# Optimization experiments

Hardware: AMD Instinct MI355X
Metric: run time of the kernel (lower is better)

## Reference

```python
import jax, jax.numpy as jnp
import numpy as np

B, G, C, H = 32, 512, 384, 768
TAU = 0.1
ITERS = 10


def _xavier(key, shape):
    fan_in, fan_out = shape
    lim = (6.0 / (fan_in + fan_out)) ** 0.5
    return jax.random.uniform(key, shape, minval=-lim, maxval=lim, dtype=jnp.float32)


def setup_inputs() -> dict:
    key = jax.random.key(0)
    ks = jax.random.split(key, 4)
    return {
        "center_coords": jax.random.normal(ks[0], (B, G, 3), dtype=jnp.float32),
        "group_features": jax.random.normal(ks[1], (B, G, C), dtype=jnp.float32),
        "W1": _xavier(ks[2], (C, H)),
        "b1": jnp.zeros((H,), jnp.float32),
        "W2": _xavier(ks[3], (H, G)),
        "b2": jnp.zeros((G,), jnp.float32),
    }


def _sinkhorn(scores):
    # scores: (B, G, G); log-space Sinkhorn row/col normalization
    log_alpha = scores / TAU
    for _ in range(ITERS):
        log_alpha = log_alpha - jax.nn.logsumexp(log_alpha, axis=-1, keepdims=True)
        log_alpha = log_alpha - jax.nn.logsumexp(log_alpha, axis=-2, keepdims=True)
    return jnp.exp(log_alpha)


def _greedy_assign(P):
    # Equivalent to torch loop: process entries in descending value order,
    # assign (row, col) if both free == repeatedly take global argmax over
    # entries with free row and free col. P: (G, G) -> perm: (G,) int32.
    g = P.shape[-1]
    flat = P.reshape(-1)

    def step(_, carry):
        row_free, col_free, assign = carry
        mask = (row_free[:, None] & col_free[None, :]).reshape(-1)
        idx = jnp.argmax(jnp.where(mask, flat, -jnp.inf))
        r = idx // g
        c = idx % g
        return (row_free.at[r].set(False), col_free.at[c].set(False), assign.at[r].set(c.astype(jnp.int32)))

    init = (jnp.ones((g,), bool), jnp.ones((g,), bool), jnp.full((g,), -1, jnp.int32))
    _, _, assign = jax.lax.fori_loop(0, g, step, init)
    return assign


def _apply_perm(data, perm):
    # reordered[new_pos] = data[orig_pos]; perm[orig_pos] = new_pos
    return jnp.zeros_like(data).at[perm].set(data)


def reference(center_coords, group_features, W1, b1, W2, b2):
    h = jax.nn.relu(jnp.einsum('bgc,ch->bgh', group_features, W1) + b1)
    scores = jnp.einsum('bgh,hk->bgk', h, W2) + b2  # (B, G, G)
    P = _sinkhorn(scores)
    perm_indices = jax.vmap(_greedy_assign)(P)  # (B, G)
    reordered_coords = jax.vmap(_apply_perm)(center_coords, perm_indices)
    reordered_feats = jax.vmap(_apply_perm)(group_features, perm_indices)
    return reordered_coords, reordered_feats, perm_indices
```

## Files before the change

### kernel.cpp

```cpp
#include <hip/hip_runtime.h>
#include <math.h>

#define NB 32
#define NG 512
#define NC 384
#define NH 768

typedef float f32x4v __attribute__((ext_vector_type(4)));
typedef __bf16 bf16_t;
typedef bf16_t bf16x8 __attribute__((ext_vector_type(8)));
typedef bf16_t bf16x4 __attribute__((ext_vector_type(4)));

#define LDSK 32

__device__ __forceinline__ void split3(float x, bf16_t& h, bf16_t& m, bf16_t& lo)
{
    h = (bf16_t)x;
    float r1 = x - (float)h;
    m = (bf16_t)r1;
    float r2 = r1 - (float)m;
    lo = (bf16_t)r2;
}

__global__ __launch_bounds__(256, 4) void gemm_bias_mfma(
    const float* __restrict__ A, const float* __restrict__ Bw,
    const float* __restrict__ bias, float* __restrict__ Co,
    int M, int N, int K, int mode)
{
    __shared__ __align__(16) bf16_t sA[3][128][LDSK];
    __shared__ __align__(16) bf16_t sB[3][64][LDSK];
    int ntiles = N >> 6;
    int bm = (blockIdx.x / ntiles) << 7;
    int bn = (blockIdx.x % ntiles) << 6;
    int t = threadIdx.x;
    int l = t & 63;
    int w = t >> 6;
    int wr = (w >> 1) << 6;
    int wc = (w & 1) << 5;
    int fr = l & 15;
    int fq = l >> 4;

    int sa_row = t >> 1;
    int sa_kh = (t & 1) << 4;
    int hsel = (sa_kh >> 4) << 2;
    int aswz = (sa_row >> 1) & 3;
    int sb_k = (t & 7) << 2;
    int sb_n = ((t >> 3) & 15) << 2;
    bool doB = t < 128;
    int bslot = (sb_k >> 2) & 3;
    int bsub = (sb_k >> 4) << 2;

    const float* apBase = A + (size_t)(bm + sa_row) * K + sa_kh;

    f32x4v acc[4][2];
#pragma unroll
    for (int i = 0; i < 4; i++)
#pragma unroll
        for (int j = 0; j < 2; j++) acc[i][j] = (f32x4v)(0.f);

    float4 q0 = *(const float4*)(apBase + 0);
    float4 q1 = *(const float4*)(apBase + 4);
    float4 q2 = *(const float4*)(apBase + 8);
    float4 q3 = *(const float4*)(apBase + 12);
    float4 bq0, bq1, bq2, bq3;
    if (doB) {
        bq0 = *(const float4*)(Bw + (size_t)(sb_k + 0) * N + bn + sb_n);
        bq1 = *(const float4*)(Bw + (size_t)(sb_k + 1) * N + bn + sb_n);
        bq2 = *(const float4*)(Bw + (size_t)(sb_k + 2) * N + bn + sb_n);
        bq3 = *(const float4*)(Bw + (size_t)(sb_k + 3) * N + bn + sb_n);
    }

    for (int kc = 0; kc < K; kc += 32) {
        __syncthreads();
        {
            float xs[16] = { q0.x, q0.y, q0.z, q0.w, q1.x, q1.y, q1.z, q1.w,
                             q2.x, q2.y, q2.z, q2.w, q3.x, q3.y, q3.z, q3.w };
            bf16_t hs[16], ms[16], ls[16];
#pragma unroll
            for (int e = 0; e < 16; e++) split3(xs[e], hs[e], ms[e], ls[e]);
#pragma unroll
            for (int qd = 0; qd < 4; qd++) {
                int col = ((qd ^ aswz) << 3) + hsel;
                *(bf16x4*)&sA[0][sa_row][col] =
                    (bf16x4){ hs[4 * qd], hs[4 * qd + 1], hs[4 * qd + 2], hs[4 * qd + 3] };
                *(bf16x4*)&sA[1][sa_row][col] =
                    (bf16x4){ ms[4 * qd], ms[4 * qd + 1], ms[4 * qd + 2], ms[4 * qd + 3] };
                *(bf16x4*)&sA[2][sa_row][col] =
                    (bf16x4){ ls[4 * qd], ls[4 * qd + 1], ls[4 * qd + 2], ls[4 * qd + 3] };
            }
        }
        if (doB) {
            float bbv[4][4] = {
                { bq0.x, bq0.y, bq0.z, bq0.w },
                { bq1.x, bq1.y, bq1.z, bq1.w },
                { bq2.x, bq2.y, bq2.z, bq2.w },
                { bq3.x, bq3.y, bq3.z, bq3.w } };
#pragma unroll
            for (int n = 0; n < 4; n++) {
                int rb = sb_n + n;
                int col = ((bslot ^ ((rb >> 1) & 3)) << 3) + bsub;
                bf16_t hb[4], mb[4], lb[4];
#pragma unroll
                for (int kk = 0; kk < 4; kk++) split3(bbv[kk][n], hb[kk], mb[kk], lb[kk]);
                *(bf16x4*)&sB[0][rb][col] = (bf16x4){ hb[0], hb[1], hb[2], hb[3] };
                *(bf16x4*)&sB[1][rb][col] = (bf16x4){ mb[0], mb[1], mb[2], mb[3] };
                *(bf16x4*)&sB[2][rb][col] = (bf16x4){ lb[0], lb[1], lb[2], lb[3] };
            }
        }
        __syncthreads();
        if (kc + 32 < K) {
            const float* ap = apBase + kc + 32;
            q0 = *(const float4*)(ap + 0);
            q1 = *(const float4*)(ap + 4);
            q2 = *(const float4*)(ap + 8);
            q3 = *(const float4*)(ap + 12);
            if (doB) {
                const float* bp = Bw + (size_t)(kc + 32 + sb_k) * N + bn + sb_n;
                bq0 = *(const float4*)(bp + 0 * N);
                bq1 = *(const float4*)(bp + 1 * N);
                bq2 = *(const float4*)(bp + 2 * N);
                bq3 = *(const float4*)(bp + 3 * N);
            }
        }
        bf16x8 afH[4], afM[4], afL[4], bfH[2], bfM[2], bfL[2];
#pragma unroll
        for (int i = 0; i < 4; i++) {
            int ra = wr + i * 16 + fr;
            int pk = ((fq ^ ((ra >> 1) & 3)) << 3);
            afH[i] = *(const bf16x8*)&sA[0][ra][pk];
            afM[i] = *(const bf16x8*)&sA[1][ra][pk];
            afL[i] = *(const bf16x8*)&sA[2][ra][pk];
        }
#pragma unroll
        for (int j = 0; j < 2; j++) {
            int rb = wc + j * 16 + fr;
            int pk = ((fq ^ ((rb >> 1) & 3)) << 3);
            bfH[j] = *(const bf16x8*)&sB[0][rb][pk];
            bfM[j] = *(const bf16x8*)&sB[1][rb][pk];
            bfL[j] = *(const bf16x8*)&sB[2][rb][pk];
        }
#pragma unroll
        for (int i = 0; i < 4; i++)
#pragma unroll
            for (int j = 0; j < 2; j++) {
                acc[i][j] = __builtin_amdgcn_mfma_f32_16x16x32_bf16(
                    afH[i], bfH[j], acc[i][j], 0, 0, 0);
                acc[i][j] = __builtin_amdgcn_mfma_f32_16x16x32_bf16(
                    afH[i], bfM[j], acc[i][j], 0, 0, 0);
                acc[i][j] = __builtin_amdgcn_mfma_f32_16x16x32_bf16(
                    afM[i], bfH[j], acc[i][j], 0, 0, 0);
                acc[i][j] = __builtin_amdgcn_mfma_f32_16x16x32_bf16(
                    afM[i], bfM[j], acc[i][j], 0, 0, 0);
                acc[i][j] = __builtin_amdgcn_mfma_f32_16x16x32_bf16(
                    afH[i], bfL[j], acc[i][j], 0, 0, 0);
                acc[i][j] = __builtin_amdgcn_mfma_f32_16x16x32_bf16(
                    afL[i], bfH[j], acc[i][j], 0, 0, 0);
            }
    }

    int orow = fq << 2;
#pragma unroll
    for (int j = 0; j < 2; j++) {
        int colg = bn + wc + j * 16 + fr;
        float bj = bias[colg];
#pragma unroll
        for (int i = 0; i < 4; i++) {
            int rowg = bm + wr + i * 16 + orow;
#pragma unroll
            for (int r = 0; r < 4; r++) {
                float val = acc[i][j][r] + bj;
                val = (mode == 0) ? fmaxf(val, 0.f) : val / 0.1f;
                Co[(size_t)(rowg + r) * N + colg] = val;
            }
        }
    }
}

#define DPP6_MAXF(x)                                                              \
    { int _t;                                                                     \
      _t = __builtin_amdgcn_update_dpp(__float_as_int(x), __float_as_int(x),      \
               0x111, 0xf, 0xf, false); x = fmaxf(x, __int_as_float(_t));         \
      _t = __builtin_amdgcn_update_dpp(__float_as_int(x), __float_as_int(x),      \
               0x112, 0xf, 0xf, false); x = fmaxf(x, __int_as_float(_t));         \
      _t = __builtin_amdgcn_update_dpp(__float_as_int(x), __float_as_int(x),      \
               0x114, 0xf, 0xf, false); x = fmaxf(x, __int_as_float(_t));         \
      _t = __builtin_amdgcn_update_dpp(__float_as_int(x), __float_as_int(x),      \
               0x118, 0xf, 0xf, false); x = fmaxf(x, __int_as_float(_t));         \
      _t = __builtin_amdgcn_update_dpp(__float_as_int(x), __float_as_int(x),      \
               0x142, 0xa, 0xf, false); x = fmaxf(x, __int_as_float(_t));         \
      _t = __builtin_amdgcn_update_dpp(__float_as_int(x), __float_as_int(x),      \
               0x143, 0xc, 0xf, false); x = fmaxf(x, __int_as_float(_t)); }

#define DPP6_ADDF(x)                                                              \
    { int _t;                                                                     \
      _t = __builtin_amdgcn_update_dpp(__float_as_int(x), __float_as_int(x),      \
               0x111, 0xf, 0xf, false); x = x + __int_as_float(_t);               \
      _t = __builtin_amdgcn_update_dpp(__float_as_int(x), __float_as_int(x),      \
               0x112, 0xf, 0xf, false); x = x + __int_as_float(_t);               \
      _t = __builtin_amdgcn_update_dpp(__float_as_int(x), __float_as_int(x),      \
               0x114, 0xf, 0xf, false); x = x + __int_as_float(_t);               \
      _t = __builtin_amdgcn_update_dpp(__float_as_int(x), __float_as_int(x),      \
               0x118, 0xf, 0xf, false); x = x + __int_as_float(_t);               \
      _t = __builtin_amdgcn_update_dpp(__float_as_int(x), __float_as_int(x),      \
               0x142, 0xa, 0xf, false); x = x + __int_as_float(_t);               \
      _t = __builtin_amdgcn_update_dpp(__float_as_int(x), __float_as_int(x),      \
               0x143, 0xc, 0xf, false); x = x + __int_as_float(_t); }

__global__ __launch_bounds__(256) void sinkhorn_iter_fused(
    const float* __restrict__ A0, float* __restrict__ uu,
    const float* __restrict__ vIn, float* __restrict__ vOut,
    const float* __restrict__ psIn, float* __restrict__ psOut, int first)
{
    int blk = blockIdx.x;
    int b = blk >> 3, rc = blk & 7;
    int t = threadIdx.x;
    int l = t & 63, w = t >> 6;
    __shared__ __align__(16) float svv[512];

    if (first) {
        svv[t] = 0.f;
        svv[256 + t] = 0.f;
    } else {
#pragma unroll
        for (int h2 = 0; h2 < 2; h2++) {
            int j = h2 * 256 + t;
            float S = 0.f;
#pragma unroll
            for (int r8 = 0; r8 < 8; r8++) S += psIn[((b << 3) + r8) * NG + j];
            float nv = vIn[(b << 9) + j] - __logf(S);
            svv[j] = nv;
            if (rc == 0) vOut[(b << 9) + j] = nv;
        }
    }
    __syncthreads();

    float4 v0 = *(const float4*)(&svv[4 * l]);
    float4 v1 = *(const float4*)(&svv[256 + 4 * l]);
    int row0 = (rc << 6) + (w << 4);
    const float* base = A0 + ((size_t)((b << 9) + row0) << 9);

    float cs0 = 0.f, cs1 = 0.f, cs2 = 0.f, cs3 = 0.f;
    float cs4 = 0.f, cs5 = 0.f, cs6 = 0.f, cs7 = 0.f;

    for (int rr = 0; rr < 16; ++rr) {
        const float* rowp = base + ((size_t)rr << 9);
        float4 a0 = *(const float4*)(rowp + 4 * l);
        float4 a1 = *(const float4*)(rowp + 256 + 4 * l);
        float x0 = a0.x + v0.x, x1 = a0.y + v0.y;
        float x2 = a0.z + v0.z, x3 = a0.w + v0.w;
        float x4 = a1.x + v1.x, x5 = a1.y + v1.y;
        float x6 = a1.z + v1.z, x7 = a1.w + v1.w;
        float m = fmaxf(fmaxf(fmaxf(x0, x1), fmaxf(x2, x3)),
                        fmaxf(fmaxf(x4, x5), fmaxf(x6, x7)));
        DPP6_MAXF(m)
        int mi = __builtin_amdgcn_readlane(__float_as_int(m), 63);
        m = __int_as_float(mi);
        float e0 = __expf(x0 - m), e1 = __expf(x1 - m);
        float e2 = __expf(x2 - m), e3 = __expf(x3 - m);
        float e4 = __expf(x4 - m), e5 = __expf(x5 - m);
        float e6 = __expf(x6 - m), e7 = __expf(x7 - m);
        float s = ((e0 + e1) + (e2 + e3)) + ((e4 + e5) + (e6 + e7));
        DPP6_ADDF(s)
        int si = __builtin_amdgcn_readlane(__float_as_int(s), 63);
        s = __int_as_float(si);
        float inv = 1.0f / s;
        cs0 += e0 * inv; cs1 += e1 * inv; cs2 += e2 * inv; cs3 += e3 * inv;
        cs4 += e4 * inv; cs5 += e5 * inv; cs6 += e6 * inv; cs7 += e7 * inv;
        if (l == 63) uu[(b << 9) + row0 + rr] = -(m + __logf(s));
    }

    __shared__ float sacc[4][512];
    float4 w0; w0.x = cs0; w0.y = cs1; w0.z = cs2; w0.w = cs3;
    float4 w1; w1.x = cs4; w1.y = cs5; w1.z = cs6; w1.w = cs7;
    *(float4*)&sacc[w][4 * l] = w0;
    *(float4*)&sacc[w][256 + 4 * l] = w1;
    __syncthreads();
    float pA = sacc[0][t] + sacc[1][t] + sacc[2][t] + sacc[3][t];
    float pB = sacc[0][256 + t] + sacc[1][256 + t] + sacc[2][256 + t] + sacc[3][256 + t];
    int o = ((b << 3) + rc) * NG;
    psOut[o + t] = pA;
    psOut[o + 256 + t] = pB;
}

__global__ __launch_bounds__(256) void col_combine_final(
    const float* __restrict__ psIn, const float* __restrict__ vIn,
    float* __restrict__ vOut)
{
    int tid = blockIdx.x * 256 + threadIdx.x;
    int b = tid >> 9, j = tid & 511;
    float S = 0.f;
#pragma unroll
    for (int r8 = 0; r8 < 8; r8++) S += psIn[((b << 3) + r8) * NG + j];
    vOut[tid] = vIn[tid] - __logf(S);
}

__device__ __forceinline__ void masked_row_argmax(
    const float* __restrict__ rowp, int l, unsigned int free8, int rr,
    float& outV, int& outF)
{
    float4 x0 = *(const float4*)(rowp + 8 * l);
    float4 x1 = *(const float4*)(rowp + 8 * l + 4);
    float q0 = (free8 & 1u)   ? x0.x : -1.0f;
    float q1 = (free8 & 2u)   ? x0.y : -1.0f;
    float q2 = (free8 & 4u)   ? x0.z : -1.0f;
    float q3 = (free8 & 8u)   ? x0.w : -1.0f;
    float q4 = (free8 & 16u)  ? x1.x : -1.0f;
    float q5 = (free8 & 32u)  ? x1.y : -1.0f;
    float q6 = (free8 & 64u)  ? x1.z : -1.0f;
    float q7 = (free8 & 128u) ? x1.w : -1.0f;
    float lm = fmaxf(fmaxf(fmaxf(q0, q1), fmaxf(q2, q3)),
                     fmaxf(fmaxf(q4, q5), fmaxf(q6, q7)));
    int sb = (rr << 9) + 8 * l;
    int lf = 0x7FFFFFFF;
    lf = (q7 == lm) ? sb + 7 : lf;
    lf = (q6 == lm) ? sb + 6 : lf;
    lf = (q5 == lm) ? sb + 5 : lf;
    lf = (q4 == lm) ? sb + 4 : lf;
    lf = (q3 == lm) ? sb + 3 : lf;
    lf = (q2 == lm) ? sb + 2 : lf;
    lf = (q1 == lm) ? sb + 1 : lf;
    lf = (q0 == lm) ? sb + 0 : lf;
    float gg = lm;
    DPP6_MAXF(gg)
    int ggi = __builtin_amdgcn_readlane(__float_as_int(gg), 63);
    float g1 = __int_as_float(ggi);
    unsigned long long tb = __ballot(lm == g1);
    int tl = __ffsll(tb) - 1;
    outV = g1;
    outF = __builtin_amdgcn_readlane(lf, tl);
}

__global__ __launch_bounds__(256) void p_rowmax(
    const float* __restrict__ A0, const float* __restrict__ uu,
    const float* __restrict__ vv, float* __restrict__ P,
    int* __restrict__ rbCr, int* __restrict__ rbCc,
    unsigned long long* __restrict__ freeRow,
    unsigned long long* __restrict__ freeCol,
    int* __restrict__ remaining)
{
    if (blockIdx.x == 0) {
        int t = threadIdx.x;
        freeRow[t] = ~0ULL;
        freeCol[t] = ~0ULL;
        if (t < NB) remaining[t] = NG;
    }
    int wrow = blockIdx.x * 4 + (threadIdx.x >> 6);
    int l = threadIdx.x & 63;
    int b = wrow >> 9;
    float ur = uu[wrow];
    const float* vb = vv + (b << 9);
    size_t ro = (size_t)wrow << 9;
    float4 a0 = *(const float4*)(A0 + ro + 8 * l);
    float4 a1 = *(const float4*)(A0 + ro + 8 * l + 4);
    float4 v0 = *(const float4*)(vb + 8 * l);
    float4 v1 = *(const float4*)(vb + 8 * l + 4);
    float p0 = expf(a0.x + ur + v0.x);
    float p1 = expf(a0.y + ur + v0.y);
    float p2 = expf(a0.z + ur + v0.z);
    float p3 = expf(a0.w + ur + v0.w);
    float p4 = expf(a1.x + ur + v1.x);
    float p5 = expf(a1.y + ur + v1.y);
    float p6 = expf(a1.z + ur + v1.z);
    float p7 = expf(a1.w + ur + v1.w);
    float4 o0; o0.x = p0; o0.y = p1; o0.z = p2; o0.w = p3;
    float4 o1; o1.x = p4; o1.y = p5; o1.z = p6; o1.w = p7;
    *(float4*)(P + ro + 8 * l) = o0;
    *(float4*)(P + ro + 8 * l + 4) = o1;
    float mv = fmaxf(fmaxf(fmaxf(p0, p1), fmaxf(p2, p3)),
                     fmaxf(fmaxf(p4, p5), fmaxf(p6, p7)));
    int cb = 8 * l;
    int f = 0x7FFFFFFF;
    f = (p7 == mv) ? cb + 7 : f;
    f = (p6 == mv) ? cb + 6 : f;
    f = (p5 == mv) ? cb + 5 : f;
    f = (p4 == mv) ? cb + 4 : f;
    f = (p3 == mv) ? cb + 3 : f;
    f = (p2 == mv) ? cb + 2 : f;
    f = (p1 == mv) ? cb + 1 : f;
    f = (p0 == mv) ? cb + 0 : f;
    float g = mv;
    DPP6_MAXF(g)
    int gi = __builtin_amdgcn_readlane(__float_as_int(g), 63);
    float gm = __int_as_float(gi);
    unsigned long long tb = __ballot(mv == gm);
    int tl = __ffsll(tb) - 1;
    int bestc = __builtin_amdgcn_readlane(f, tl);
    if (l == 0) { rbCr[wrow] = bestc; rbCc[wrow] = -1; }
}

__global__ __launch_bounds__(512) void mutual_round(
    const float* __restrict__ P, int* __restrict__ rbCr, int* __restrict__ rbCc,
    unsigned long long* __restrict__ freeRow,
    unsigned long long* __restrict__ freeCol,
    int* __restrict__ remaining, int* __restrict__ permInt)
{
    int b = blockIdx.x;
    if (remaining[b] == 0) return;
    int t = threadIdx.x;
    int l = t & 63;
    int w = t >> 6;
    const float* Pb = P + (size_t)b * NG * NG;

    __shared__ unsigned int fr[16], fc[16];
    __shared__ int sRC[NG];
    __shared__ int sCC[NG];
    __shared__ int freeList[NG];
    __shared__ int dirtyRows[NG];
    __shared__ int nFree, nDirtyRow, takeCnt;
    __shared__ int wCnt[8], wOff[8];

    if (t < 8) {
        unsigned long long x = freeRow[b * 8 + t];
        fr[2 * t] = (unsigned)x; fr[2 * t + 1] = (unsigned)(x >> 32);
    } else if (t < 16) {
        int i = t - 8;
        unsigned long long x = freeCol[b * 8 + i];
        fc[2 * i] = (unsigned)x; fc[2 * i + 1] = (unsigned)(x >> 32);
    }
    sRC[t] = rbCr[(b << 9) + t];
    sCC[t] = rbCc[(b << 9) + t];
    if (t == 0) { nDirtyRow = 0; takeCnt = 0; }
    __syncthreads();

    bool isFree = (fr[t >> 5] >> (t & 31)) & 1u;
    unsigned long long bm = __ballot(isFree);
    if (l == 0) wCnt[w] = __popcll(bm);
    if (isFree) {
        int c = sRC[t];
        if (!((fc[c >> 5] >> (c & 31)) & 1u)) {
            int d = atomicAdd(&nDirtyRow, 1);
            dirtyRows[d] = t;
        }
    }
    __syncthreads();
    if (t == 0) {
        int s = 0;
#pragma unroll
        for (int i = 0; i < 8; i++) { wOff[i] = s; s += wCnt[i]; }
        nFree = s;
    }
    __syncthreads();
    if (isFree) {
        int rank = __popcll(bm & ((1ULL << l) - 1ULL));
        freeList[wOff[w] + rank] = t;
    }
    __syncthreads();

    int nd = nDirtyRow;
    for (int d = w; d < nd; d += 8) {
        int r = dirtyRows[d];
        unsigned int free8 = (fc[l >> 2] >> ((l & 3) * 8)) & 0xFFu;
        float nv; int nf;
        masked_row_argmax(Pb + ((size_t)r << 9), l, free8, r, nv, nf);
        if (l == 0) {
            int c = nf & 511;
            sRC[r] = c;
            rbCr[(b << 9) + r] = c;
        }
    }
    __syncthreads();

    bool colFree = (fc[t >> 5] >> (t & 31)) & 1u;
    int cachedR = sCC[t];
    bool colDirty = colFree &&
        (cachedR < 0 || !((fr[cachedR >> 5] >> (cachedR & 31)) & 1u));
    if (colDirty) {
        float best = -1.f; int bestr = 0x7FFFFFFF;
        int nf2 = nFree;
        int i = 0;
        for (; i + 4 <= nf2; i += 4) {
            int r0 = freeList[i], r1 = freeList[i + 1];
            int r2 = freeList[i + 2], r3 = freeList[i + 3];
            float v0 = Pb[((size_t)r0 << 9) + t];
            float v1 = Pb[((size_t)r1 << 9) + t];
            float v2 = Pb[((size_t)r2 << 9) + t];
            float v3 = Pb[((size_t)r3 << 9) + t];
            if (v0 > best) { best = v0; bestr = r0; }
            if (v1 > best) { best = v1; bestr = r1; }
            if (v2 > best) { best = v2; bestr = r2; }
            if (v3 > best) { best = v3; bestr = r3; }
        }
        for (; i < nf2; ++i) {
            int ri = freeList[i];
            float vv2 = Pb[((size_t)ri << 9) + t];
            if (vv2 > best) { best = vv2; bestr = ri; }
        }
        sCC[t] = bestr;
        rbCc[(b << 9) + t] = bestr;
    }
    __syncthreads();

    if (colFree) {
        int r = sCC[t];
        if (r >= 0 && r < NG && sRC[r] == t) {
            permInt[(b << 9) + r] = t;
            atomicAnd(&fr[r >> 5], ~(1u << (r & 31)));
            atomicAnd(&fc[t >> 5], ~(1u << (t & 31)));
            atomicAdd(&takeCnt, 1);
        }
    }
    __syncthreads();
    if (t < 8) {
        freeRow[b * 8 + t] =
            ((unsigned long long)fr[2 * t + 1] << 32) | fr[2 * t];
    } else if (t < 16) {
        int i = t - 8;
        freeCol[b * 8 + i] =
            ((unsigned long long)fc[2 * i + 1] << 32) | fc[2 * i];
    }
    if (t == 0) remaining[b] = remaining[b] - takeCnt;
}

__global__ __launch_bounds__(64) void greedy_cleanup(
    const float* __restrict__ P,
    const unsigned long long* __restrict__ freeRow,
    const unsigned long long* __restrict__ freeCol,
    const int* __restrict__ remaining, int* __restrict__ permInt)
{
    int b = blockIdx.x;
    if (remaining[b] == 0) return;
    int l = threadIdx.x;
    const float* Pb = P + (size_t)b * NG * NG;

    unsigned long long wR = freeRow[b * 8 + (l >> 3)];
    unsigned int myRows = (unsigned int)((wR >> ((l & 7) * 8)) & 0xFF);
    unsigned long long wC = freeCol[b * 8 + (l >> 3)];
    unsigned int free8 = (unsigned int)((wC >> ((l & 7) * 8)) & 0xFF);

    float rv[8]; int rf[8];
#pragma unroll
    for (int k = 0; k < 8; k++) { rv[k] = -1.f; rf[k] = 0x7FFFFFFF; }

    int dmk = (int)myRows;
    unsigned long long act = __ballot(dmk != 0);
    while (act) {
        int src = __ffsll(act) - 1;
        int kk = __ffs(__builtin_amdgcn_readlane(dmk, src)) - 1;
        if (l == src) dmk &= ~(1 << kk);
        int rr = (src << 3) + kk;
        float nv; int nf;
        masked_row_argmax(Pb + ((size_t)rr << 9), l, free8, rr, nv, nf);
        bool upd = (l == src);
        rv[0] = (upd && kk == 0) ? nv : rv[0]; rf[0] = (upd && kk == 0) ? nf : rf[0];
        rv[1] = (upd && kk == 1) ? nv : rv[1]; rf[1] = (upd && kk == 1) ? nf : rf[1];
        rv[2] = (upd && kk == 2) ? nv : rv[2]; rf[2] = (upd && kk == 2) ? nf : rf[2];
        rv[3] = (upd && kk == 3) ? nv : rv[3]; rf[3] = (upd && kk == 3) ? nf : rf[3];
        rv[4] = (upd && kk == 4) ? nv : rv[4]; rf[4] = (upd && kk == 4) ? nf : rf[4];
        rv[5] = (upd && kk == 5) ? nv : rv[5]; rf[5] = (upd && kk == 5) ? nf : rf[5];
        rv[6] = (upd && kk == 6) ? nv : rv[6]; rf[6] = (upd && kk == 6) ? nf : rf[6];
        rv[7] = (upd && kk == 7) ? nv : rv[7]; rf[7] = (upd && kk == 7) ? nf : rf[7];
        act = __ballot(dmk != 0);
    }

    for (int step = 0; step < NG; ++step) {
        float mv = fmaxf(fmaxf(fmaxf(rv[0], rv[1]), fmaxf(rv[2], rv[3])),
                         fmaxf(fmaxf(rv[4], rv[5]), fmaxf(rv[6], rv[7])));
        int f = 0x7FFFFFFF;
        f = (rv[7] == mv) ? rf[7] : f;
        f = (rv[6] == mv) ? rf[6] : f;
        f = (rv[5] == mv) ? rf[5] : f;
        f = (rv[4] == mv) ? rf[4] : f;
        f = (rv[3] == mv) ? rf[3] : f;
        f = (rv[2] == mv) ? rf[2] : f;
        f = (rv[1] == mv) ? rf[1] : f;
        f = (rv[0] == mv) ? rf[0] : f;
        float g = mv;
        DPP6_MAXF(g)
        int gi = __builtin_amdgcn_readlane(__float_as_int(g), 63);
        float gm = __int_as_float(gi);
        if (gm < 0.f) break;
        unsigned long long tb = __ballot(mv == gm);
        int tl = __ffsll(tb) - 1;
        int bestf = __builtin_amdgcn_readlane(f, tl);
        int r = bestf >> 9, c = bestf & 511;
        if (l == 0) permInt[(b << 9) + r] = c;
        if (l == (c >> 3)) free8 &= ~(1u << (c & 7));
        int rl = r - (l << 3);
        int dm2 = 0;
#pragma unroll
        for (int k = 0; k < 8; k++) {
            bool alive = rv[k] >= 0.f;
            bool cm = ((rf[k] ^ c) & 511) == 0;
            bool taken = (rl == k);
            if (taken) rv[k] = -1.f;
            dm2 |= (alive && cm && !taken) ? (1 << k) : 0;
        }
        unsigned long long act2 = __ballot(dm2 != 0);
        while (act2) {
            int src = __ffsll(act2) - 1;
            int kk = __ffs(__builtin_amdgcn_readlane(dm2, src)) - 1;
            if (l == src) dm2 &= ~(1 << kk);
            int rr = (src << 3) + kk;
            float nv; int nf;
            masked_row_argmax(Pb + ((size_t)rr << 9), l, free8, rr, nv, nf);
            bool upd = (l == src);
            rv[0] = (upd && kk == 0) ? nv : rv[0]; rf[0] = (upd && kk == 0) ? nf : rf[0];
            rv[1] = (upd && kk == 1) ? nv : rv[1]; rf[1] = (upd && kk == 1) ? nf : rf[1];
            rv[2] = (upd && kk == 2) ? nv : rv[2]; rf[2] = (upd && kk == 2) ? nf : rf[2];
            rv[3] = (upd && kk == 3) ? nv : rv[3]; rf[3] = (upd && kk == 3) ? nf : rf[3];
            rv[4] = (upd && kk == 4) ? nv : rv[4]; rf[4] = (upd && kk == 4) ? nf : rf[4];
            rv[5] = (upd && kk == 5) ? nv : rv[5]; rf[5] = (upd && kk == 5) ? nf : rf[5];
            rv[6] = (upd && kk == 6) ? nv : rv[6]; rf[6] = (upd && kk == 6) ? nf : rf[6];
            rv[7] = (upd && kk == 7) ? nv : rv[7]; rf[7] = (upd && kk == 7) ? nf : rf[7];
            act2 = __ballot(dm2 != 0);
        }
    }
}

__global__ void scatter_all(const float* __restrict__ coords,
    const float* __restrict__ feats, const int* __restrict__ perm,
    float* __restrict__ dstCoords, float* __restrict__ dstFeats,
    float* __restrict__ permF)
{
    int tid = blockIdx.x * 256 + threadIdx.x;
    int rc = tid / 96;
    int q = tid - rc * 96;
    int b = rc >> 9;
    int p = perm[rc];
    const float4* s4 = (const float4*)(feats + (size_t)rc * NC);
    float4* d4 = (float4*)(dstFeats + ((size_t)(b << 9) + p) * NC);
    d4[q] = s4[q];
    if (q == 0) {
        permF[rc] = (float)p;
        size_t so = (size_t)rc * 3;
        size_t dd = ((size_t)(b << 9) + p) * 3;
        dstCoords[dd] = coords[so];
        dstCoords[dd + 1] = coords[so + 1];
        dstCoords[dd + 2] = coords[so + 2];
    }
}

extern "C" void kernel_launch(void* const* d_in, const int* in_sizes, int n_in,
                              void* d_out, int out_size, void* d_ws, size_t ws_size,
                              hipStream_t stream)
{
    const float* coords = (const float*)d_in[0];
    const float* feats  = (const float*)d_in[1];
    const float* W1 = (const float*)d_in[2];
    const float* b1 = (const float*)d_in[3];
    const float* W2 = (const float*)d_in[4];
    const float* b2 = (const float*)d_in[5];

    float* out = (float*)d_out;
    float* outCoords = out;
    float* outFeats  = out + (size_t)NB * NG * 3;
    float* outPerm   = out + (size_t)NB * NG * 3 + (size_t)NB * NG * NC;

    float* ws = (float*)d_ws;
    float* h   = ws;
    float* A0  = h + (size_t)NB * NG * NH;
    float* u   = A0 + (size_t)NB * NG * NG;
    float* vA  = u + NB * NG;
    float* ps0 = vA + NB * NG;
    float* ps1 = ps0 + NB * 8 * NG;
    int* rbCr  = (int*)(ps1 + NB * 8 * NG);
    int* rbCc  = rbCr + NB * NG;
    unsigned long long* freeRow = (unsigned long long*)(rbCc + NB * NG);
    unsigned long long* freeCol = freeRow + NB * 8;
    int* remaining = (int*)(freeCol + NB * 8);
    int* permInt   = remaining + 32;
    float* vB  = (float*)(permInt + NB * NG);

    const int M = NB * NG;

    gemm_bias_mfma<<<dim3((M / 128) * (NH / 64)), 256, 0, stream>>>(
        feats, W1, b1, h, M, NH, NC, 0);
    gemm_bias_mfma<<<dim3((M / 128) * (NG / 64)), 256, 0, stream>>>(
        h, W2, b2, A0, M, NG, NH, 1);

    hipMemsetAsync(vA, 0, (size_t)NB * NG * sizeof(float), stream);

    float* pbuf[2] = { ps0, ps1 };
    for (int i = 1; i <= 10; ++i) {
        const float* vin = (i % 2 == 0) ? vA : vB;
        float* vout      = (i % 2 == 0) ? vB : vA;
        const float* pin = pbuf[i & 1];
        float* pout      = pbuf[(i - 1) & 1];
        sinkhorn_iter_fused<<<dim3(NB * 8), 256, 0, stream>>>(
            A0, u, vin, vout, pin, pout, (i == 1) ? 1 : 0);
    }
    col_combine_final<<<dim3(M / 256), 256, 0, stream>>>(pbuf[1], vB, vA);

    float* P = h;
    p_rowmax<<<dim3(M / 4), 256, 0, stream>>>(A0, u, vA, P, rbCr, rbCc,
                                              freeRow, freeCol, remaining);

    for (int r = 0; r < 6; ++r)
        mutual_round<<<dim3(NB), 512, 0, stream>>>(P, rbCr, rbCc, freeRow,
                                                   freeCol, remaining, permInt);

    greedy_cleanup<<<dim3(NB), 64, 0, stream>>>(P, freeRow, freeCol,
                                                remaining, permInt);

    scatter_all<<<dim3((NB * NG * 96) / 256), 256, 0, stream>>>(
        coords, feats, permInt, outCoords, outFeats, outPerm);
}
```

Measured before the change: 403.0 us.

## Pre-split weights into swizzled bf16 planes and shrink GEMM tile to 64x64

Adds a presplit_W kernel that converts W1/W2 once per call into three bf16 planes (hi/mid/lo) already in the swizzled LDS layout. The GEMM then copies B tiles straight into shared memory instead of loading fp32 and splitting them in every block. The M tile also shrinks from 128 to 64 rows, giving twice as many blocks with fewer accumulators each. The cost is two extra small launches, extra workspace for the planes, and more redundant reads of A across column tiles.

```diff
diff --git a/kernel.cpp b/kernel.cpp
--- a/kernel.cpp
+++ b/kernel.cpp
@@ -10,8 +10,6 @@
 typedef __bf16 bf16_t;
 typedef bf16_t bf16x8 __attribute__((ext_vector_type(8)));
 typedef bf16_t bf16x4 __attribute__((ext_vector_type(4)));
-
-#define LDSK 32
 
 __device__ __forceinline__ void split3(float x, bf16_t& h, bf16_t& m, bf16_t& lo)
 {
@@ -22,111 +20,111 @@
     lo = (bf16_t)r2;
 }
 
+__global__ __launch_bounds__(256) void presplit_W(
+    const float* __restrict__ W, bf16_t* __restrict__ planeB, int K, int N)
+{
+    int tid = blockIdx.x * 256 + threadIdx.x;
+    int nkc = K >> 5;
+    if (tid >= nkc * N) return;
+    int kc = tid / N;
+    int col = tid - kc * N;
+    bf16x8 rh[4], rm[4], rl[4];
+#pragma unroll
+    for (int k = 0; k < 32; k++) {
+        float x = W[(size_t)(kc * 32 + k) * N + col];
+        bf16_t h, m, lo;
+        split3(x, h, m, lo);
+        const int s = (k >> 2) & 3;
+        const int sub = ((k >> 4) << 2) + (k & 3);
+        rh[s][sub] = h; rm[s][sub] = m; rl[s][sub] = lo;
+    }
+    int swz = (col >> 1) & 3;
+    size_t b0 = ((size_t)(kc * 3 + 0) * N + col) * 32;
+    size_t b1 = ((size_t)(kc * 3 + 1) * N + col) * 32;
+    size_t b2 = ((size_t)(kc * 3 + 2) * N + col) * 32;
+#pragma unroll
+    for (int s = 0; s < 4; s++) {
+        int d = (s ^ swz) << 3;
+        *(bf16x8*)&planeB[b0 + d] = rh[s];
+        *(bf16x8*)&planeB[b1 + d] = rm[s];
+        *(bf16x8*)&planeB[b2 + d] = rl[s];
+    }
+}
+
 __global__ __launch_bounds__(256, 4) void gemm_bias_mfma(
-    const float* __restrict__ A, const float* __restrict__ Bw,
+    const float* __restrict__ A, const bf16_t* __restrict__ planeB,
     const float* __restrict__ bias, float* __restrict__ Co,
     int M, int N, int K, int mode)
 {
-    __shared__ __align__(16) bf16_t sA[3][128][LDSK];
-    __shared__ __align__(16) bf16_t sB[3][64][LDSK];
+    __shared__ __align__(16) bf16_t sA[3][64][32];
+    __shared__ __align__(16) bf16_t sB[3][64][32];
     int ntiles = N >> 6;
-    int bm = (blockIdx.x / ntiles) << 7;
+    int bm = (blockIdx.x / ntiles) << 6;
     int bn = (blockIdx.x % ntiles) << 6;
     int t = threadIdx.x;
-    int l = t & 63;
-    int w = t >> 6;
-    int wr = (w >> 1) << 6;
+    int l = t & 63, w = t >> 6;
+    int wr = (w >> 1) << 5;
     int wc = (w & 1) << 5;
     int fr = l & 15;
     int fq = l >> 4;
 
-    int sa_row = t >> 1;
-    int sa_kh = (t & 1) << 4;
-    int hsel = (sa_kh >> 4) << 2;
+    int sa_row = t >> 2;
+    int sa_k0 = (t & 3) << 3;
+    int qA = (sa_k0 >> 2) & 3;
+    int hsel = (sa_k0 & 16) ? 4 : 0;
     int aswz = (sa_row >> 1) & 3;
-    int sb_k = (t & 7) << 2;
-    int sb_n = ((t >> 3) & 15) << 2;
-    bool doB = t < 128;
-    int bslot = (sb_k >> 2) & 3;
-    int bsub = (sb_k >> 4) << 2;
-
-    const float* apBase = A + (size_t)(bm + sa_row) * K + sa_kh;
-
-    f32x4v acc[4][2];
-#pragma unroll
-    for (int i = 0; i < 4; i++)
+    int colQ0 = ((qA ^ aswz) << 3) + hsel;
+    int colQ1 = (((qA + 1) ^ aswz) << 3) + hsel;
+    const float* apBase = A + (size_t)(bm + sa_row) * K + sa_k0;
+
+    int sbc = t >> 2;
+    int sbs = (t & 3) << 3;
+
+    f32x4v acc[2][2];
+#pragma unroll
+    for (int i = 0; i < 2; i++)
 #pragma unroll
         for (int j = 0; j < 2; j++) acc[i][j] = (f32x4v)(0.f);
 
-    float4 q0 = *(const float4*)(apBase + 0);
-    float4 q1 = *(const float4*)(apBase + 4);
-    float4 q2 = *(const float4*)(apBase + 8);
-    float4 q3 = *(const float4*)(apBase + 12);
-    float4 bq0, bq1, bq2, bq3;
-    if (doB) {
-        bq0 = *(const float4*)(Bw + (size_t)(sb_k + 0) * N + bn + sb_n);
-        bq1 = *(const float4*)(Bw + (size_t)(sb_k + 1) * N + bn + sb_n);
-        bq2 = *(const float4*)(Bw + (size_t)(sb_k + 2) * N + bn + sb_n);
-        bq3 = *(const float4*)(Bw + (size_t)(sb_k + 3) * N + bn + sb_n);
-    }
+    float4 qa0 = *(const float4*)(apBase);
+    float4 qa1 = *(const float4*)(apBase + 4);
+    bf16x8 pb0 = *(const bf16x8*)&planeB[((size_t)0 * N + bn + sbc) * 32 + sbs];
+    bf16x8 pb1 = *(const bf16x8*)&planeB[((size_t)1 * N + bn + sbc) * 32 + sbs];
+    bf16x8 pb2 = *(const bf16x8*)&planeB[((size_t)2 * N + bn + sbc) * 32 + sbs];
 
     for (int kc = 0; kc < K; kc += 32) {
+        int kci = kc >> 5;
         __syncthreads();
         {
-            float xs[16] = { q0.x, q0.y, q0.z, q0.w, q1.x, q1.y, q1.z, q1.w,
-                             q2.x, q2.y, q2.z, q2.w, q3.x, q3.y, q3.z, q3.w };
-            bf16_t hs[16], ms[16], ls[16];
-#pragma unroll
-            for (int e = 0; e < 16; e++) split3(xs[e], hs[e], ms[e], ls[e]);
-#pragma unroll
-            for (int qd = 0; qd < 4; qd++) {
-                int col = ((qd ^ aswz) << 3) + hsel;
-                *(bf16x4*)&sA[0][sa_row][col] =
-                    (bf16x4){ hs[4 * qd], hs[4 * qd + 1], hs[4 * qd + 2], hs[4 * qd + 3] };
-                *(bf16x4*)&sA[1][sa_row][col] =
-                    (bf16x4){ ms[4 * qd], ms[4 * qd + 1], ms[4 * qd + 2], ms[4 * qd + 3] };
-                *(bf16x4*)&sA[2][sa_row][col] =
-                    (bf16x4){ ls[4 * qd], ls[4 * qd + 1], ls[4 * qd + 2], ls[4 * qd + 3] };
-            }
-        }
-        if (doB) {
-            float bbv[4][4] = {
-                { bq0.x, bq0.y, bq0.z, bq0.w },
-                { bq1.x, bq1.y, bq1.z, bq1.w },
-                { bq2.x, bq2.y, bq2.z, bq2.w },
-                { bq3.x, bq3.y, bq3.z, bq3.w } };
-#pragma unroll
-            for (int n = 0; n < 4; n++) {
-                int rb = sb_n + n;
-                int col = ((bslot ^ ((rb >> 1) & 3)) << 3) + bsub;
-                bf16_t hb[4], mb[4], lb[4];
-#pragma unroll
-                for (int kk = 0; kk < 4; kk++) split3(bbv[kk][n], hb[kk], mb[kk], lb[kk]);
-                *(bf16x4*)&sB[0][rb][col] = (bf16x4){ hb[0], hb[1], hb[2], hb[3] };
-                *(bf16x4*)&sB[1][rb][col] = (bf16x4){ mb[0], mb[1], mb[2], mb[3] };
-                *(bf16x4*)&sB[2][rb][col] = (bf16x4){ lb[0], lb[1], lb[2], lb[3] };
-            }
-        }
+            float xs[8] = { qa0.x, qa0.y, qa0.z, qa0.w,
+                            qa1.x, qa1.y, qa1.z, qa1.w };
+            bf16_t hs[8], ms[8], ls[8];
+#pragma unroll
+            for (int e = 0; e < 8; e++) split3(xs[e], hs[e], ms[e], ls[e]);
+            *(bf16x4*)&sA[0][sa_row][colQ0] = (bf16x4){ hs[0], hs[1], hs[2], hs[3] };
+            *(bf16x4*)&sA[0][sa_row][colQ1] = (bf16x4){ hs[4], hs[5], hs[6], hs[7] };
+            *(bf16x4*)&sA[1][sa_row][colQ0] = (bf16x4){ ms[0], ms[1], ms[2], ms[3] };
+            *(bf16x4*)&sA[1][sa_row][colQ1] = (bf16x4){ ms[4], ms[5], ms[6], ms[7] };
+            *(bf16x4*)&sA[2][sa_row][colQ0] = (bf16x4){ ls[0], ls[1], ls[2], ls[3] };
+            *(bf16x4*)&sA[2][sa_row][colQ1] = (bf16x4){ ls[4], ls[5], ls[6], ls[7] };
+        }
+        *(bf16x8*)&sB[0][sbc][sbs] = pb0;
+        *(bf16x8*)&sB[1][sbc][sbs] = pb1;
+        *(bf16x8*)&sB[2][sbc][sbs] = pb2;
         __syncthreads();
         if (kc + 32 < K) {
             const float* ap = apBase + kc + 32;
-            q0 = *(const float4*)(ap + 0);
-            q1 = *(const float4*)(ap + 4);
-            q2 = *(const float4*)(ap + 8);
-            q3 = *(const float4*)(ap + 12);
-            if (doB) {
-                const float* bp = Bw + (size_t)(kc + 32 + sb_k) * N + bn + sb_n;
-                bq0 = *(const float4*)(bp + 0 * N);
-                bq1 = *(const float4*)(bp + 1 * N);
-                bq2 = *(const float4*)(bp + 2 * N);
-                bq3 = *(const float4*)(bp + 3 * N);
-            }
-        }
-        bf16x8 afH[4], afM[4], afL[4], bfH[2], bfM[2], bfL[2];
-#pragma unroll
-        for (int i = 0; i < 4; i++) {
+            qa0 = *(const float4*)(ap);
+            qa1 = *(const float4*)(ap + 4);
+            pb0 = *(const bf16x8*)&planeB[((size_t)((kci + 1) * 3 + 0) * N + bn + sbc) * 32 + sbs];
+            pb1 = *(const bf16x8*)&planeB[((size_t)((kci + 1) * 3 + 1) * N + bn + sbc) * 32 + sbs];
+            pb2 = *(const bf16x8*)&planeB[((size_t)((kci + 1) * 3 + 2) * N + bn + sbc) * 32 + sbs];
+        }
+        bf16x8 afH[2], afM[2], afL[2], bfH[2], bfM[2], bfL[2];
+#pragma unroll
+        for (int i = 0; i < 2; i++) {
             int ra = wr + i * 16 + fr;
-            int pk = ((fq ^ ((ra >> 1) & 3)) << 3);
+            int pk = (fq ^ ((ra >> 1) & 3)) << 3;
             afH[i] = *(const bf16x8*)&sA[0][ra][pk];
             afM[i] = *(const bf16x8*)&sA[1][ra][pk];
             afL[i] = *(const bf16x8*)&sA[2][ra][pk];
@@ -134,13 +132,13 @@
 #pragma unroll
         for (int j = 0; j < 2; j++) {
             int rb = wc + j * 16 + fr;
-            int pk = ((fq ^ ((rb >> 1) & 3)) << 3);
+            int pk = (fq ^ ((rb >> 1) & 3)) << 3;
             bfH[j] = *(const bf16x8*)&sB[0][rb][pk];
             bfM[j] = *(const bf16x8*)&sB[1][rb][pk];
             bfL[j] = *(const bf16x8*)&sB[2][rb][pk];
         }
 #pragma unroll
-        for (int i = 0; i < 4; i++)
+        for (int i = 0; i < 2; i++)
 #pragma unroll
             for (int j = 0; j < 2; j++) {
                 acc[i][j] = __builtin_amdgcn_mfma_f32_16x16x32_bf16(
@@ -164,7 +162,7 @@
         int colg = bn + wc + j * 16 + fr;
         float bj = bias[colg];
 #pragma unroll
-        for (int i = 0; i < 4; i++) {
+        for (int i = 0; i < 2; i++) {
             int rowg = bm + wr + i * 16 + orow;
 #pragma unroll
             for (int r = 0; r < 4; r++) {
@@ -660,13 +658,18 @@
     int* remaining = (int*)(freeCol + NB * 8);
     int* permInt   = remaining + 32;
     float* vB  = (float*)(permInt + NB * NG);
+    bf16_t* pB1 = (bf16_t*)(vB + NB * NG);
+    bf16_t* pB2 = pB1 + 12 * 3 * NH * 32;
 
     const int M = NB * NG;
 
-    gemm_bias_mfma<<<dim3((M / 128) * (NH / 64)), 256, 0, stream>>>(
-        feats, W1, b1, h, M, NH, NC, 0);
-    gemm_bias_mfma<<<dim3((M / 128) * (NG / 64)), 256, 0, stream>>>(
-        h, W2, b2, A0, M, NG, NH, 1);
+    presplit_W<<<dim3((12 * NH + 255) / 256), 256, 0, stream>>>(W1, pB1, NC, NH);
+    presplit_W<<<dim3((24 * NG + 255) / 256), 256, 0, stream>>>(W2, pB2, NH, NG);
+
+    gemm_bias_mfma<<<dim3((M / 64) * (NH / 64)), 256, 0, stream>>>(
+        feats, pB1, b1, h, M, NH, NC, 0);
+    gemm_bias_mfma<<<dim3((M / 64) * (NG / 64)), 256, 0, stream>>>(
+        h, pB2, b2, A0, M, NG, NH, 1);
 
     hipMemsetAsync(vA, 0, (size_t)NB * NG * sizeof(float), stream);
 
```

Measured after the change: 409.8 us. Within noise of the previous version (+1.7%).
